# Performance work log

Measured on AMD Instinct MI355X. Metric: run time of the kernel, lower is better.

Reference implementation:

```python
import jax, jax.numpy as jnp
import numpy as np
import math

EPS = 1e-12  # F.normalize default eps

def _l2_normalize(x):
    n = jnp.sqrt(jnp.sum(x * x, axis=-1, keepdims=True))
    return x / jnp.maximum(n, EPS)

def setup_inputs() -> dict:
    key = jax.random.key(0)
    k1, k2 = jax.random.split(key)
    B, F, C = 16384, 1024, 1000
    features = jax.random.normal(k1, (B, F), dtype=jnp.float32)
    prototypes = jax.random.normal(k2, (C, F), dtype=jnp.float32)
    distance_scale = jnp.ones((1,), dtype=jnp.float32)
    temperature = jnp.ones((1,), dtype=jnp.float32)
    return {"features": features, "prototypes": prototypes,
            "distance_scale": distance_scale, "temperature": temperature}

def reference(features, prototypes, distance_scale, temperature):
    # L2-normalize both sides (F.normalize, p=2, eps=1e-12)
    f = _l2_normalize(features)      # [B, F]
    p = _l2_normalize(prototypes)    # [C, F]
    # Pairwise Euclidean distance. For unit vectors ||f-p||^2 = 2 - 2 f.p,
    # clamped at 0 for numerical safety; then / sqrt(2).
    sim = jnp.einsum('bf,cf->bc', f, p)                  # [B, C]
    sq = jnp.maximum(2.0 - 2.0 * sim, 0.0)
    distances = jnp.sqrt(sq) / jnp.float32(math.sqrt(2.0))
    iso = jnp.abs(distance_scale) * distances            # [B, C]
    logits = -(iso + jnp.mean(iso, axis=1, keepdims=True))
    return logits / temperature
```

## Files before the change

kernel.cpp:

```cpp
#include <hip/hip_runtime.h>
#include <hip/hip_bf16.h>
#include <math.h>

#define B_ROWS 16384
#define C_COLS 1000
#define C_PAD  1024
#define FDIM   1024

typedef __attribute__((ext_vector_type(8))) short bf16x8;
typedef __attribute__((ext_vector_type(4))) float f32x4;

#define GLD_LDS(gp, lp) __builtin_amdgcn_global_load_lds( \
    (__attribute__((address_space(1))) void*)(gp),        \
    (__attribute__((address_space(3))) void*)(lp), 16, 0, 0)

__global__ __launch_bounds__(256) void normalize_rows(
    const float* __restrict__ in, __hip_bfloat16* __restrict__ out, int nrows_valid)
{
    const int lane = threadIdx.x & 63;
    const int wave = threadIdx.x >> 6;
    const int row  = blockIdx.x * 4 + wave;
    __hip_bfloat16* orow = out + (size_t)row * FDIM;

    if (row >= nrows_valid) {
        ushort4 z = make_ushort4(0, 0, 0, 0);
        #pragma unroll
        for (int c = 0; c < 4; ++c) ((ushort4*)orow)[lane + c * 64] = z;
        return;
    }

    const float4* rp = (const float4*)(in + (size_t)row * FDIM);
    float4 v[4];
    float ss = 0.0f;
    #pragma unroll
    for (int c = 0; c < 4; ++c) {
        v[c] = rp[lane + c * 64];
        ss += v[c].x * v[c].x + v[c].y * v[c].y + v[c].z * v[c].z + v[c].w * v[c].w;
    }
    #pragma unroll
    for (int off = 1; off < 64; off <<= 1) ss += __shfl_xor(ss, off, 64);
    const float inv = 1.0f / sqrtf(fmaxf(ss, 1e-24f));

    #pragma unroll
    for (int c = 0; c < 4; ++c) {
        __hip_bfloat16 o[4];
        o[0] = __float2bfloat16(v[c].x * inv);
        o[1] = __float2bfloat16(v[c].y * inv);
        o[2] = __float2bfloat16(v[c].z * inv);
        o[3] = __float2bfloat16(v[c].w * inv);
        ((ushort4*)orow)[lane + c * 64] = *(ushort4*)o;
    }
}

__global__ __launch_bounds__(256) void gemm_dist(
    const __hip_bfloat16* __restrict__ A,
    const __hip_bfloat16* __restrict__ Bp,
    __hip_bfloat16* __restrict__ D,
    float* __restrict__ rowsum)
{
    __shared__ __hip_bfloat16 As[128 * 64];
    __shared__ __hip_bfloat16 Bs[128 * 64];

    const int tid  = threadIdx.x;
    const int lane = tid & 63;
    const int wave = tid >> 6;

    const int id  = blockIdx.x;
    const int xcd = id & 7;
    const int seq = id >> 3;
    const int bn  = seq & 7;
    const int bm  = xcd * 16 + (seq >> 3);

    const int waveM = (wave >> 1) * 64;
    const int waveN = (wave & 1) * 64;

    f32x4 acc[4][4] = {};

    const int srow  = lane >> 3;
    const int sksub = (lane & 7) ^ (srow & 7);
    const __hip_bfloat16* Abase = A  + ((size_t)(bm * 128) + srow) * FDIM + sksub * 8;
    const __hip_bfloat16* Bbase = Bp + ((size_t)(bn * 128) + srow) * FDIM + sksub * 8;

    #pragma unroll 1
    for (int k0 = 0; k0 < FDIM; k0 += 64) {
        __syncthreads();
        #pragma unroll
        for (int c4 = 0; c4 < 4; ++c4) {
            const int chunk = wave * 4 + c4;
            GLD_LDS(Abase + (size_t)(chunk * 8) * FDIM + k0, &As[chunk * 512]);
            GLD_LDS(Bbase + (size_t)(chunk * 8) * FDIM + k0, &Bs[chunk * 512]);
        }
        __syncthreads();

        #pragma unroll
        for (int h = 0; h < 2; ++h) {
            bf16x8 a[4], b[4];
            const int q = h * 4 + (lane >> 4);
            #pragma unroll
            for (int mt = 0; mt < 4; ++mt) {
                const int R = waveM + mt * 16 + (lane & 15);
                a[mt] = *(const bf16x8*)&As[R * 64 + ((q ^ (R & 7)) * 8)];
            }
            #pragma unroll
            for (int nt = 0; nt < 4; ++nt) {
                const int R = waveN + nt * 16 + (lane & 15);
                b[nt] = *(const bf16x8*)&Bs[R * 64 + ((q ^ (R & 7)) * 8)];
            }
            #pragma unroll
            for (int mt = 0; mt < 4; ++mt)
                #pragma unroll
                for (int nt = 0; nt < 4; ++nt)
                    acc[mt][nt] = __builtin_amdgcn_mfma_f32_16x16x32_bf16(a[mt], b[nt], acc[mt][nt], 0, 0, 0);
        }
    }

    const int row0 = bm * 128 + waveM;
    const int col0 = bn * 128 + waveN;
    #pragma unroll
    for (int mt = 0; mt < 4; ++mt) {
        #pragma unroll
        for (int r = 0; r < 4; ++r) {
            const int row = row0 + mt * 16 + (lane >> 4) * 4 + r;
            float part = 0.0f;
            #pragma unroll
            for (int nt = 0; nt < 4; ++nt) {
                const int col = col0 + nt * 16 + (lane & 15);
                const float sim = acc[mt][nt][r];
                const float dv = sqrtf(fmaxf(1.0f - sim, 0.0f));
                if (col < C_COLS) {
                    D[(size_t)row * C_COLS + col] = __float2bfloat16(dv);
                    part += dv;
                }
            }
            part += __shfl_xor(part, 1, 64);
            part += __shfl_xor(part, 2, 64);
            part += __shfl_xor(part, 4, 64);
            part += __shfl_xor(part, 8, 64);
            if ((lane & 15) == 0) atomicAdd(&rowsum[row], part);
        }
    }
}

__global__ __launch_bounds__(256) void finalize(
    const __hip_bfloat16* __restrict__ D, const float* __restrict__ rowsum,
    const float* __restrict__ scale, const float* __restrict__ temp,
    float* __restrict__ out)
{
    const size_t i = (size_t)blockIdx.x * 256 + threadIdx.x;
    const float a = -fabsf(scale[0]) / temp[0];
    const int row = (int)((i * 8) / C_COLS);
    const float m = rowsum[row] * (1.0f / (float)C_COLS);

    const bf16x8 dv = *(const bf16x8*)(D + i * 8);
    const __hip_bfloat16* dp = (const __hip_bfloat16*)&dv;
    float4 o0, o1;
    o0.x = a * (__bfloat162float(dp[0]) + m);
    o0.y = a * (__bfloat162float(dp[1]) + m);
    o0.z = a * (__bfloat162float(dp[2]) + m);
    o0.w = a * (__bfloat162float(dp[3]) + m);
    o1.x = a * (__bfloat162float(dp[4]) + m);
    o1.y = a * (__bfloat162float(dp[5]) + m);
    o1.z = a * (__bfloat162float(dp[6]) + m);
    o1.w = a * (__bfloat162float(dp[7]) + m);
    ((float4*)out)[i * 2]     = o0;
    ((float4*)out)[i * 2 + 1] = o1;
}

extern "C" void kernel_launch(void* const* d_in, const int* in_sizes, int n_in,
                              void* d_out, int out_size, void* d_ws, size_t ws_size,
                              hipStream_t stream)
{
    const float* features = (const float*)d_in[0];
    const float* protos   = (const float*)d_in[1];
    const float* dscale   = (const float*)d_in[2];
    const float* temp     = (const float*)d_in[3];
    float* out = (float*)d_out;

    char* ws = (char*)d_ws;
    __hip_bfloat16* fb = (__hip_bfloat16*)ws;
    __hip_bfloat16* pb = (__hip_bfloat16*)(ws + 33554432);
    __hip_bfloat16* D  = (__hip_bfloat16*)(ws + 35651584);
    float* rowsum      = (float*)(ws + 68419584);

    hipMemsetAsync(rowsum, 0, B_ROWS * sizeof(float), stream);

    normalize_rows<<<B_ROWS / 4, 256, 0, stream>>>(features, fb, B_ROWS);
    normalize_rows<<<C_PAD / 4,  256, 0, stream>>>(protos,   pb, C_COLS);

    gemm_dist<<<1024, 256, 0, stream>>>(fb, pb, D, rowsum);

    finalize<<<(B_ROWS * C_COLS / 8) / 256, 256, 0, stream>>>(D, rowsum, dscale, temp, out);
}
```

Measured before the change: 186.1 us.

## Fuse finalize into GEMM via last-block counters and merge normalize launches

Combines the two row-normalization launches into a single kernel that dispatches on block index. Removes the separate finalize kernel by having the last GEMM block to finish each 128-row slab (tracked with an atomic counter) apply the mean and scale to that slab. This cuts launch overhead and lets the epilogue overlap with other blocks' GEMM work. The risk is tail imbalance, since one block per slab now does all of that slab's finalize work.

```diff
diff --git a/kernel.cpp b/kernel.cpp
--- a/kernel.cpp
+++ b/kernel.cpp
@@ -6,6 +6,8 @@
 #define C_COLS 1000
 #define C_PAD  1024
 #define FDIM   1024
+#define NBM    128
+#define FBLKS  4096
 
 typedef __attribute__((ext_vector_type(8))) short bf16x8;
 typedef __attribute__((ext_vector_type(4))) float f32x4;
@@ -14,15 +16,24 @@
     (__attribute__((address_space(1))) void*)(gp),        \
     (__attribute__((address_space(3))) void*)(lp), 16, 0, 0)
 
-__global__ __launch_bounds__(256) void normalize_rows(
-    const float* __restrict__ in, __hip_bfloat16* __restrict__ out, int nrows_valid)
+__global__ __launch_bounds__(256) void normalize_all(
+    const float* __restrict__ feat, const float* __restrict__ prot,
+    __hip_bfloat16* __restrict__ fb, __hip_bfloat16* __restrict__ pb)
 {
     const int lane = threadIdx.x & 63;
     const int wave = threadIdx.x >> 6;
-    const int row  = blockIdx.x * 4 + wave;
+
+    const float* in;
+    __hip_bfloat16* out;
+    int row, nvalid;
+    if (blockIdx.x < FBLKS) {
+        row = blockIdx.x * 4 + wave;  in = feat; out = fb; nvalid = B_ROWS;
+    } else {
+        row = (blockIdx.x - FBLKS) * 4 + wave;  in = prot; out = pb; nvalid = C_COLS;
+    }
     __hip_bfloat16* orow = out + (size_t)row * FDIM;
 
-    if (row >= nrows_valid) {
+    if (row >= nvalid) {
         ushort4 z = make_ushort4(0, 0, 0, 0);
         #pragma unroll
         for (int c = 0; c < 4; ++c) ((ushort4*)orow)[lane + c * 64] = z;
@@ -56,10 +67,14 @@
     const __hip_bfloat16* __restrict__ A,
     const __hip_bfloat16* __restrict__ Bp,
     __hip_bfloat16* __restrict__ D,
-    float* __restrict__ rowsum)
+    float* __restrict__ rowsum,
+    int* __restrict__ cnt,
+    const float* __restrict__ scale, const float* __restrict__ temp,
+    float* __restrict__ out)
 {
     __shared__ __hip_bfloat16 As[128 * 64];
     __shared__ __hip_bfloat16 Bs[128 * 64];
+    __shared__ int amLast;
 
     const int tid  = threadIdx.x;
     const int lane = tid & 63;
@@ -139,31 +154,35 @@
             if ((lane & 15) == 0) atomicAdd(&rowsum[row], part);
         }
     }
-}
-
-__global__ __launch_bounds__(256) void finalize(
-    const __hip_bfloat16* __restrict__ D, const float* __restrict__ rowsum,
-    const float* __restrict__ scale, const float* __restrict__ temp,
-    float* __restrict__ out)
-{
-    const size_t i = (size_t)blockIdx.x * 256 + threadIdx.x;
+
+    __threadfence();
+    __syncthreads();
+    if (tid == 0) amLast = (atomicAdd(&cnt[bm], 1) == 7);
+    __syncthreads();
+    if (!amLast) return;
+    __threadfence();
+
     const float a = -fabsf(scale[0]) / temp[0];
-    const int row = (int)((i * 8) / C_COLS);
-    const float m = rowsum[row] * (1.0f / (float)C_COLS);
-
-    const bf16x8 dv = *(const bf16x8*)(D + i * 8);
-    const __hip_bfloat16* dp = (const __hip_bfloat16*)&dv;
-    float4 o0, o1;
-    o0.x = a * (__bfloat162float(dp[0]) + m);
-    o0.y = a * (__bfloat162float(dp[1]) + m);
-    o0.z = a * (__bfloat162float(dp[2]) + m);
-    o0.w = a * (__bfloat162float(dp[3]) + m);
-    o1.x = a * (__bfloat162float(dp[4]) + m);
-    o1.y = a * (__bfloat162float(dp[5]) + m);
-    o1.z = a * (__bfloat162float(dp[6]) + m);
-    o1.w = a * (__bfloat162float(dp[7]) + m);
-    ((float4*)out)[i * 2]     = o0;
-    ((float4*)out)[i * 2 + 1] = o1;
+    for (int g = tid; g < 128 * 125; g += 256) {
+        const int r   = g / 125;
+        const int c8  = g - r * 125;
+        const int row = bm * 128 + r;
+        const float m = rowsum[row] * (1.0f / (float)C_COLS);
+        const bf16x8 dv = *(const bf16x8*)(D + (size_t)row * C_COLS + c8 * 8);
+        const __hip_bfloat16* dp = (const __hip_bfloat16*)&dv;
+        float4 o0, o1;
+        o0.x = a * (__bfloat162float(dp[0]) + m);
+        o0.y = a * (__bfloat162float(dp[1]) + m);
+        o0.z = a * (__bfloat162float(dp[2]) + m);
+        o0.w = a * (__bfloat162float(dp[3]) + m);
+        o1.x = a * (__bfloat162float(dp[4]) + m);
+        o1.y = a * (__bfloat162float(dp[5]) + m);
+        o1.z = a * (__bfloat162float(dp[6]) + m);
+        o1.w = a * (__bfloat162float(dp[7]) + m);
+        float4* op = (float4*)(out + (size_t)row * C_COLS + c8 * 8);
+        op[0] = o0;
+        op[1] = o1;
+    }
 }
 
 extern "C" void kernel_launch(void* const* d_in, const int* in_sizes, int n_in,
@@ -181,13 +200,11 @@
     __hip_bfloat16* pb = (__hip_bfloat16*)(ws + 33554432);
     __hip_bfloat16* D  = (__hip_bfloat16*)(ws + 35651584);
     float* rowsum      = (float*)(ws + 68419584);
-
-    hipMemsetAsync(rowsum, 0, B_ROWS * sizeof(float), stream);
-
-    normalize_rows<<<B_ROWS / 4, 256, 0, stream>>>(features, fb, B_ROWS);
-    normalize_rows<<<C_PAD / 4,  256, 0, stream>>>(protos,   pb, C_COLS);
-
-    gemm_dist<<<1024, 256, 0, stream>>>(fb, pb, D, rowsum);
-
-    finalize<<<(B_ROWS * C_COLS / 8) / 256, 256, 0, stream>>>(D, rowsum, dscale, temp, out);
+    int*   cnt         = (int*)  (ws + 68485120);
+
+    hipMemsetAsync(rowsum, 0, B_ROWS * sizeof(float) + NBM * sizeof(int), stream);
+
+    normalize_all<<<FBLKS + C_PAD / 4, 256, 0, stream>>>(features, protos, fb, pb);
+
+    gemm_dist<<<1024, 256, 0, stream>>>(fb, pb, D, rowsum, cnt, dscale, temp, out);
 }
```

Result: slower. 391.2 us (+110.2%).

## Use 256x128 GEMM tiles with 32x32 MFMA and merge normalize launches

Applied to the files above, without the earlier changes.

The GEMM tile grows from 128x128 to 256x128, so each wave computes a 128x64 sub-tile with 32x32x16 bf16 MFMA instructions instead of 16x16x32, and the grid shrinks to 512 blocks. This raises arithmetic intensity per LDS read and cuts redundant loads of B tiles, at the cost of more LDS (48KB) and accumulator registers, with launch_bounds hinting two blocks per CU. The two normalization launches are merged into one kernel to save a launch. The epilogue row mapping and reduction are adapted to the 32x32 MFMA output layout.

```diff
diff --git a/kernel.cpp b/kernel.cpp
--- a/kernel.cpp
+++ b/kernel.cpp
@@ -6,23 +6,33 @@
 #define C_COLS 1000
 #define C_PAD  1024
 #define FDIM   1024
-
-typedef __attribute__((ext_vector_type(8))) short bf16x8;
-typedef __attribute__((ext_vector_type(4))) float f32x4;
+#define FBLKS  4096
+
+typedef __attribute__((ext_vector_type(8)))  short bf16x8;
+typedef __attribute__((ext_vector_type(16))) float f32x16;
 
 #define GLD_LDS(gp, lp) __builtin_amdgcn_global_load_lds( \
     (__attribute__((address_space(1))) void*)(gp),        \
     (__attribute__((address_space(3))) void*)(lp), 16, 0, 0)
 
-__global__ __launch_bounds__(256) void normalize_rows(
-    const float* __restrict__ in, __hip_bfloat16* __restrict__ out, int nrows_valid)
+__global__ __launch_bounds__(256) void normalize_all(
+    const float* __restrict__ feat, const float* __restrict__ prot,
+    __hip_bfloat16* __restrict__ fb, __hip_bfloat16* __restrict__ pb)
 {
     const int lane = threadIdx.x & 63;
     const int wave = threadIdx.x >> 6;
-    const int row  = blockIdx.x * 4 + wave;
+
+    const float* in;
+    __hip_bfloat16* out;
+    int row, nvalid;
+    if (blockIdx.x < FBLKS) {
+        row = blockIdx.x * 4 + wave;  in = feat; out = fb; nvalid = B_ROWS;
+    } else {
+        row = (blockIdx.x - FBLKS) * 4 + wave;  in = prot; out = pb; nvalid = C_COLS;
+    }
     __hip_bfloat16* orow = out + (size_t)row * FDIM;
 
-    if (row >= nrows_valid) {
+    if (row >= nvalid) {
         ushort4 z = make_ushort4(0, 0, 0, 0);
         #pragma unroll
         for (int c = 0; c < 4; ++c) ((ushort4*)orow)[lane + c * 64] = z;
@@ -52,13 +62,13 @@
     }
 }
 
-__global__ __launch_bounds__(256) void gemm_dist(
+__global__ __launch_bounds__(256, 2) void gemm_dist(
     const __hip_bfloat16* __restrict__ A,
     const __hip_bfloat16* __restrict__ Bp,
     __hip_bfloat16* __restrict__ D,
     float* __restrict__ rowsum)
 {
-    __shared__ __hip_bfloat16 As[128 * 64];
+    __shared__ __hip_bfloat16 As[256 * 64];
     __shared__ __hip_bfloat16 Bs[128 * 64];
 
     const int tid  = threadIdx.x;
@@ -69,62 +79,59 @@
     const int xcd = id & 7;
     const int seq = id >> 3;
     const int bn  = seq & 7;
-    const int bm  = xcd * 16 + (seq >> 3);
-
-    const int waveM = (wave >> 1) * 64;
+    const int bmg = xcd * 8 + (seq >> 3);
+
+    const int waveM = (wave >> 1) * 128;
     const int waveN = (wave & 1) * 64;
 
-    f32x4 acc[4][4] = {};
+    f32x16 acc[4][2] = {};
 
     const int srow  = lane >> 3;
     const int sksub = (lane & 7) ^ (srow & 7);
-    const __hip_bfloat16* Abase = A  + ((size_t)(bm * 128) + srow) * FDIM + sksub * 8;
-    const __hip_bfloat16* Bbase = Bp + ((size_t)(bn * 128) + srow) * FDIM + sksub * 8;
+    const __hip_bfloat16* Abase = A  + ((size_t)(bmg * 256) + srow) * FDIM + sksub * 8;
+    const __hip_bfloat16* Bbase = Bp + ((size_t)(bn  * 128) + srow) * FDIM + sksub * 8;
 
     #pragma unroll 1
     for (int k0 = 0; k0 < FDIM; k0 += 64) {
         __syncthreads();
         #pragma unroll
-        for (int c4 = 0; c4 < 4; ++c4) {
-            const int chunk = wave * 4 + c4;
-            GLD_LDS(Abase + (size_t)(chunk * 8) * FDIM + k0, &As[chunk * 512]);
-            GLD_LDS(Bbase + (size_t)(chunk * 8) * FDIM + k0, &Bs[chunk * 512]);
+        for (int j = 0; j < 12; ++j) {
+            const int c = wave * 12 + j;
+            if (c < 32) GLD_LDS(Abase + (size_t)(c * 8) * FDIM + k0, &As[c * 512]);
+            else        GLD_LDS(Bbase + (size_t)((c - 32) * 8) * FDIM + k0, &Bs[(c - 32) * 512]);
         }
         __syncthreads();
 
         #pragma unroll
-        for (int h = 0; h < 2; ++h) {
-            bf16x8 a[4], b[4];
-            const int q = h * 4 + (lane >> 4);
+        for (int s = 0; s < 4; ++s) {
+            const int oct = s * 2 + (lane >> 5);
+            bf16x8 b[2];
+            #pragma unroll
+            for (int nt = 0; nt < 2; ++nt) {
+                const int R = waveN + nt * 32 + (lane & 31);
+                b[nt] = *(const bf16x8*)&Bs[R * 64 + ((oct ^ (R & 7)) * 8)];
+            }
             #pragma unroll
             for (int mt = 0; mt < 4; ++mt) {
-                const int R = waveM + mt * 16 + (lane & 15);
-                a[mt] = *(const bf16x8*)&As[R * 64 + ((q ^ (R & 7)) * 8)];
+                const int R = waveM + mt * 32 + (lane & 31);
+                const bf16x8 a = *(const bf16x8*)&As[R * 64 + ((oct ^ (R & 7)) * 8)];
+                acc[mt][0] = __builtin_amdgcn_mfma_f32_32x32x16_bf16(a, b[0], acc[mt][0], 0, 0, 0);
+                acc[mt][1] = __builtin_amdgcn_mfma_f32_32x32x16_bf16(a, b[1], acc[mt][1], 0, 0, 0);
             }
-            #pragma unroll
-            for (int nt = 0; nt < 4; ++nt) {
-                const int R = waveN + nt * 16 + (lane & 15);
-                b[nt] = *(const bf16x8*)&Bs[R * 64 + ((q ^ (R & 7)) * 8)];
-            }
-            #pragma unroll
-            for (int mt = 0; mt < 4; ++mt)
-                #pragma unroll
-                for (int nt = 0; nt < 4; ++nt)
-                    acc[mt][nt] = __builtin_amdgcn_mfma_f32_16x16x32_bf16(a[mt], b[nt], acc[mt][nt], 0, 0, 0);
         }
     }
 
-    const int row0 = bm * 128 + waveM;
+    const int row0 = bmg * 256 + waveM;
     const int col0 = bn * 128 + waveN;
     #pragma unroll
     for (int mt = 0; mt < 4; ++mt) {
         #pragma unroll
-        for (int r = 0; r < 4; ++r) {
-            const int row = row0 + mt * 16 + (lane >> 4) * 4 + r;
+        for (int r = 0; r < 16; ++r) {
+            const int row = row0 + mt * 32 + (r & 3) + 8 * (r >> 2) + 4 * (lane >> 5);
             float part = 0.0f;
             #pragma unroll
-            for (int nt = 0; nt < 4; ++nt) {
-                const int col = col0 + nt * 16 + (lane & 15);
+            for (int nt = 0; nt < 2; ++nt) {
+                const int col = col0 + nt * 32 + (lane & 31);
                 const float sim = acc[mt][nt][r];
                 const float dv = sqrtf(fmaxf(1.0f - sim, 0.0f));
                 if (col < C_COLS) {
@@ -136,7 +143,8 @@
             part += __shfl_xor(part, 2, 64);
             part += __shfl_xor(part, 4, 64);
             part += __shfl_xor(part, 8, 64);
-            if ((lane & 15) == 0) atomicAdd(&rowsum[row], part);
+            part += __shfl_xor(part, 16, 64);
+            if ((lane & 31) == 0) atomicAdd(&rowsum[row], part);
         }
     }
 }
@@ -184,10 +192,9 @@
 
     hipMemsetAsync(rowsum, 0, B_ROWS * sizeof(float), stream);
 
-    normalize_rows<<<B_ROWS / 4, 256, 0, stream>>>(features, fb, B_ROWS);
-    normalize_rows<<<C_PAD / 4,  256, 0, stream>>>(protos,   pb, C_COLS);
-
-    gemm_dist<<<1024, 256, 0, stream>>>(fb, pb, D, rowsum);
+    normalize_all<<<FBLKS + C_PAD / 4, 256, 0, stream>>>(features, protos, fb, pb);
+
+    gemm_dist<<<512, 256, 0, stream>>>(fb, pb, D, rowsum);
 
     finalize<<<(B_ROWS * C_COLS / 8) / 256, 256, 0, stream>>>(D, rowsum, dscale, temp, out);
 }
```

Measured after the change: 188.6 us. Within noise of the previous version (+1.3%).

## Double-buffer GEMM LDS tiles with BK=32 and merge normalize launches

Applied to the files above, without the earlier changes.

The GEMM main loop now uses two LDS buffers of 32-wide K tiles. It issues the global-to-LDS loads for the next tile before running the MFMAs on the current one, so there is one barrier per iteration instead of two and load latency overlaps with compute. The LDS swizzle is reworked for the narrower tile. The two normalization launches are merged into one kernel that dispatches on block index, which saves a launch. The trade-offs are more iterations with less work per barrier, and the hazard that a prefetch may overwrite a buffer still being read if the barrier placement is wrong.

```diff
diff --git a/kernel.cpp b/kernel.cpp
--- a/kernel.cpp
+++ b/kernel.cpp
@@ -6,6 +6,7 @@
 #define C_COLS 1000
 #define C_PAD  1024
 #define FDIM   1024
+#define FBLKS  4096
 
 typedef __attribute__((ext_vector_type(8))) short bf16x8;
 typedef __attribute__((ext_vector_type(4))) float f32x4;
@@ -14,15 +15,24 @@
     (__attribute__((address_space(1))) void*)(gp),        \
     (__attribute__((address_space(3))) void*)(lp), 16, 0, 0)
 
-__global__ __launch_bounds__(256) void normalize_rows(
-    const float* __restrict__ in, __hip_bfloat16* __restrict__ out, int nrows_valid)
+__global__ __launch_bounds__(256) void normalize_all(
+    const float* __restrict__ feat, const float* __restrict__ prot,
+    __hip_bfloat16* __restrict__ fb, __hip_bfloat16* __restrict__ pb)
 {
     const int lane = threadIdx.x & 63;
     const int wave = threadIdx.x >> 6;
-    const int row  = blockIdx.x * 4 + wave;
+
+    const float* in;
+    __hip_bfloat16* out;
+    int row, nvalid;
+    if (blockIdx.x < FBLKS) {
+        row = blockIdx.x * 4 + wave;  in = feat; out = fb; nvalid = B_ROWS;
+    } else {
+        row = (blockIdx.x - FBLKS) * 4 + wave;  in = prot; out = pb; nvalid = C_COLS;
+    }
     __hip_bfloat16* orow = out + (size_t)row * FDIM;
 
-    if (row >= nrows_valid) {
+    if (row >= nvalid) {
         ushort4 z = make_ushort4(0, 0, 0, 0);
         #pragma unroll
         for (int c = 0; c < 4; ++c) ((ushort4*)orow)[lane + c * 64] = z;
@@ -58,8 +68,8 @@
     __hip_bfloat16* __restrict__ D,
     float* __restrict__ rowsum)
 {
-    __shared__ __hip_bfloat16 As[128 * 64];
-    __shared__ __hip_bfloat16 Bs[128 * 64];
+    __shared__ __hip_bfloat16 As[2][128 * 32];
+    __shared__ __hip_bfloat16 Bs[2][128 * 32];
 
     const int tid  = threadIdx.x;
     const int lane = tid & 63;
@@ -76,42 +86,45 @@
 
     f32x4 acc[4][4] = {};
 
-    const int srow  = lane >> 3;
-    const int sksub = (lane & 7) ^ (srow & 7);
-    const __hip_bfloat16* Abase = A  + ((size_t)(bm * 128) + srow) * FDIM + sksub * 8;
-    const __hip_bfloat16* Bbase = Bp + ((size_t)(bn * 128) + srow) * FDIM + sksub * 8;
-
-    #pragma unroll 1
-    for (int k0 = 0; k0 < FDIM; k0 += 64) {
+    const int srow = lane >> 2;
+    const int sq   = (lane & 3) ^ ((srow >> 1) & 3);
+    const __hip_bfloat16* Abase = A  + ((size_t)(bm * 128) + wave * 32 + srow) * FDIM + sq * 8;
+    const __hip_bfloat16* Bbase = Bp + ((size_t)(bn * 128) + wave * 32 + srow) * FDIM + sq * 8;
+
+    #define STAGE(koff, b) do {                                              \
+        GLD_LDS(Abase + (size_t)(koff),             &As[b][wave * 1024]);        \
+        GLD_LDS(Abase + (size_t)(koff) + 16 * FDIM, &As[b][wave * 1024 + 512]);  \
+        GLD_LDS(Bbase + (size_t)(koff),             &Bs[b][wave * 1024]);        \
+        GLD_LDS(Bbase + (size_t)(koff) + 16 * FDIM, &Bs[b][wave * 1024 + 512]);  \
+    } while (0)
+
+    STAGE(0, 0);
+    __syncthreads();
+
+    const int q = lane >> 4;
+    #pragma unroll 2
+    for (int k = 0; k < 32; ++k) {
+        const int cur = k & 1;
+        if (k < 31) STAGE((k + 1) * 32, cur ^ 1);
+
+        bf16x8 a[4], b[4];
+        #pragma unroll
+        for (int mt = 0; mt < 4; ++mt) {
+            const int R = waveM + mt * 16 + (lane & 15);
+            a[mt] = *(const bf16x8*)&As[cur][R * 32 + ((q ^ ((R >> 1) & 3)) * 8)];
+        }
+        #pragma unroll
+        for (int nt = 0; nt < 4; ++nt) {
+            const int R = waveN + nt * 16 + (lane & 15);
+            b[nt] = *(const bf16x8*)&Bs[cur][R * 32 + ((q ^ ((R >> 1) & 3)) * 8)];
+        }
+        #pragma unroll
+        for (int mt = 0; mt < 4; ++mt)
+            #pragma unroll
+            for (int nt = 0; nt < 4; ++nt)
+                acc[mt][nt] = __builtin_amdgcn_mfma_f32_16x16x32_bf16(a[mt], b[nt], acc[mt][nt], 0, 0, 0);
+
         __syncthreads();
-        #pragma unroll
-        for (int c4 = 0; c4 < 4; ++c4) {
-            const int chunk = wave * 4 + c4;
-            GLD_LDS(Abase + (size_t)(chunk * 8) * FDIM + k0, &As[chunk * 512]);
-            GLD_LDS(Bbase + (size_t)(chunk * 8) * FDIM + k0, &Bs[chunk * 512]);
-        }
-        __syncthreads();
-
-        #pragma unroll
-        for (int h = 0; h < 2; ++h) {
-            bf16x8 a[4], b[4];
-            const int q = h * 4 + (lane >> 4);
-            #pragma unroll
-            for (int mt = 0; mt < 4; ++mt) {
-                const int R = waveM + mt * 16 + (lane & 15);
-                a[mt] = *(const bf16x8*)&As[R * 64 + ((q ^ (R & 7)) * 8)];
-            }
-            #pragma unroll
-            for (int nt = 0; nt < 4; ++nt) {
-                const int R = waveN + nt * 16 + (lane & 15);
-                b[nt] = *(const bf16x8*)&Bs[R * 64 + ((q ^ (R & 7)) * 8)];
-            }
-            #pragma unroll
-            for (int mt = 0; mt < 4; ++mt)
-                #pragma unroll
-                for (int nt = 0; nt < 4; ++nt)
-                    acc[mt][nt] = __builtin_amdgcn_mfma_f32_16x16x32_bf16(a[mt], b[nt], acc[mt][nt], 0, 0, 0);
-        }
     }
 
     const int row0 = bm * 128 + waveM;
@@ -184,8 +197,7 @@
 
     hipMemsetAsync(rowsum, 0, B_ROWS * sizeof(float), stream);
 
-    normalize_rows<<<B_ROWS / 4, 256, 0, stream>>>(features, fb, B_ROWS);
-    normalize_rows<<<C_PAD / 4,  256, 0, stream>>>(protos,   pb, C_COLS);
+    normalize_all<<<FBLKS + C_PAD / 4, 256, 0, stream>>>(features, protos, fb, pb);
 
     gemm_dist<<<1024, 256, 0, stream>>>(fb, pb, D, rowsum);
 
```

Result: slower. 192.8 us (+3.6%).
